# Performance work log

Hardware: AMD Instinct MI355X
Metric: run time of the kernel (lower is better)

The kernel has to match this reference:

```python
import jax, jax.numpy as jnp
import numpy as np

S, B, C = 56, 32, 1024
T = 48
H = 1024          # hidden_size_decoder (== context_size C)
EMB = 512
RANK = 128
VOCAB = 32000


def setup_inputs() -> dict:
    key = jax.random.key(0)
    ks = jax.random.split(key, 16)
    w = 0.05
    inp = {
        "encoded": jax.random.normal(ks[0], (S, B, C), jnp.float32),
        "encoder_state": jax.random.normal(ks[1], (2, B, H), jnp.float32) * 0.1,
        "tgt_tokens": jax.random.randint(ks[2], (B, T), 0, VOCAB),
        "enc_lens": jax.random.randint(ks[3], (B,), S // 2, S + 1).astype(jnp.int32),
        "tgt_lens": jax.random.randint(ks[4], (B,), T // 2, T + 1).astype(jnp.int32),
        "E": jax.random.normal(ks[5], (VOCAB, RANK), jnp.float32) * w,
        "P": jax.random.normal(ks[6], (RANK, EMB), jnp.float32) * w,
        "W0": jax.random.normal(ks[7], (EMB + C, 4 * H), jnp.float32) * w,
        "U0": jax.random.normal(ks[8], (H, 4 * H), jnp.float32) * w,
        "b0": jnp.zeros((4 * H,), jnp.float32),
        "W1": jax.random.normal(ks[9], (H, 4 * H), jnp.float32) * w,
        "U1": jax.random.normal(ks[10], (H, 4 * H), jnp.float32) * w,
        "b1": jnp.zeros((4 * H,), jnp.float32),
        "Wo": jax.random.normal(ks[11], (H + C, EMB), jnp.float32) * w,
        "bo": jnp.zeros((EMB,), jnp.float32),
    }
    return inp


def _lstm_cell(x, h, c, W, U, b):
    gates = x @ W + h @ U + b                      # [B, 4H]
    i, f, g, o = jnp.split(gates, 4, axis=-1)      # torch LSTMCell gate order
    c_new = jax.nn.sigmoid(f) * c + jax.nn.sigmoid(i) * jnp.tanh(g)
    h_new = jax.nn.sigmoid(o) * jnp.tanh(c_new)
    return h_new, c_new


def reference(encoded, encoder_state, tgt_tokens, enc_lens, tgt_lens,
              E, P, W0, U0, b0, W1, U1, b1, Wo, bo):
    # encoded: [S, B, C] (padded encoder outputs), encoder_state: [L=2, B, H]
    enc_b = jnp.transpose(encoded, (1, 0, 2))                 # [B, S, C]
    enc_mask = jnp.arange(S)[None, :] >= enc_lens[:, None]    # [B, S] True = pad

    # factorized embedding lookup (dropout p=0)
    emb = (E[tgt_tokens] @ P)                                 # [B, T, EMB]
    emb_t = jnp.transpose(emb, (1, 0, 2))[: T - 1]            # [T-1, B, EMB]

    h0 = encoder_state                                        # [2, B, H]
    c0 = jnp.zeros_like(encoder_state)
    ctx0 = jnp.zeros((B, C), encoded.dtype)

    def step(carry, x_emb):
        h, c, ctx = carry
        x = jnp.concatenate([x_emb, ctx], axis=-1)            # [B, EMB+C]
        h0n, c0n = _lstm_cell(x, h[0], c[0], W0, U0, b0)
        h1n, c1n = _lstm_cell(h0n, h[1], c[1], W1, U1, b1)
        query = h1n                                           # no context projection
        scores = jnp.einsum("bsc,bc->bs", enc_b, query)       # [B, S]
        scores = jnp.where(enc_mask, -jnp.inf, scores)
        p_att = jax.nn.softmax(scores, axis=-1)
        ctx_new = jnp.einsum("bs,bsc->bc", p_att, enc_b)      # [B, C]
        return (jnp.stack([h0n, h1n]), jnp.stack([c0n, c1n]), ctx_new), (h1n, ctx_new)

    _, (decs, ctxs) = jax.lax.scan(step, (h0, c0, ctx0), emb_t)  # each [T-1, B, *]

    feats = jnp.concatenate([decs, ctxs], axis=-1)            # [T-1, B, H+C]
    hproj = jnp.tanh(feats @ Wo + bo)                          # [T-1, B, EMB]
    logits = (hproj @ P.T) @ E.T                               # [T-1, B, VOCAB]

    labels = tgt_tokens[:, 1:].T                               # [T-1, B]
    logp = jax.nn.log_softmax(logits, axis=-1)
    nll = -jnp.take_along_axis(logp, labels[..., None], axis=-1)[..., 0]
    valid = jnp.arange(T - 1)[:, None] < (tgt_lens[None, :] - 1)  # step t predicts token t+1
    loss = jnp.sum(jnp.where(valid, nll, 0.0))                 # CrossEntropyLoss(reduction='sum')
    return loss
```

## Files before the change

kernel.cpp:

```cpp
#include <hip/hip_runtime.h>
#include <math.h>

#define S_   56
#define B_   32
#define C_   1024
#define T_   48
#define TS   47
#define H_   1024
#define EMB_ 512
#define RANK_ 128
#define VOCAB_ 32000
#define G4   4096
#define NBLK 256

using bf16x8 = __attribute__((ext_vector_type(8))) __bf16;
using f32x4  = __attribute__((ext_vector_type(4))) float;

__device__ __forceinline__ float sigmoidf_(float x){ return 1.0f/(1.0f+expf(-x)); }
__device__ __forceinline__ float b2f(__bf16 x){ return (float)x; }
__device__ __forceinline__ f32x4 z4(){ f32x4 z = {0.f,0.f,0.f,0.f}; return z; }

#define AG __HIP_MEMORY_SCOPE_AGENT
__device__ __forceinline__ void stc_u64(void* p, unsigned long long v){
  __hip_atomic_store((unsigned long long*)p, v, __ATOMIC_RELAXED, AG);
}
__device__ __forceinline__ void stc_bf16(__bf16* p, __bf16 v){
  union { __bf16 b; unsigned short s; } t; t.b = v;
  __hip_atomic_store((unsigned short*)p, t.s, __ATOMIC_RELAXED, AG);
}

struct RedShared {
  float red[4][2][16][18];
};
struct AttnShared {
  union { float hS[1024]; float cred[3][128][8]; } u;
  float sS[64];
  float pS[64];
};
union alignas(16) SharedU { RedShared r; AttnShared a; };

__device__ __forceinline__ void bar_arrive(unsigned* bars, int bi, unsigned e){
  asm volatile("s_waitcnt vmcnt(0)" ::: "memory");
  __syncthreads();
  if (threadIdx.x == 0){
    unsigned* grp = bars + 32*(1 + (bi & 15));
    unsigned old = __hip_atomic_fetch_add(grp, 1u, __ATOMIC_RELAXED, AG);
    if (old == 16u*e - 1u)
      __hip_atomic_fetch_add(bars, 1u, __ATOMIC_RELAXED, AG);
  }
}
__device__ __forceinline__ void bar_wait(unsigned* bars, unsigned e){
  if (threadIdx.x == 0){
    while (__hip_atomic_load(bars, __ATOMIC_RELAXED, AG) < 16u*e)
      __builtin_amdgcn_s_sleep(1);
  }
  __syncthreads();
  asm volatile("" ::: "memory");
}
__device__ __forceinline__ void flag_wait(unsigned* cc, unsigned tgt){
  if (threadIdx.x == 0){
    while (__hip_atomic_load(cc, __ATOMIC_RELAXED, AG) < tgt)
      __builtin_amdgcn_s_sleep(1);
  }
  __syncthreads();
  asm volatile("" ::: "memory");
}

__global__ void k_init(const float* __restrict__ es, __bf16* h0bm1, __bf16* fm1,
                       unsigned* bars){
  int i = blockIdx.x*blockDim.x + threadIdx.x;
  if (i < 32*H_){
    int b = i >> 10, j = i & 1023;
    h0bm1[(size_t)b*1024 + j]       = (__bf16)es[i];
    fm1[(size_t)b*2048 + j]         = (__bf16)es[32*H_ + i];
    fm1[(size_t)b*2048 + 1024 + j]  = (__bf16)0.0f;
  }
  if (i < 1024) bars[i] = 0u;
}

__global__ void k_cvt(const float* __restrict__ src, __bf16* __restrict__ dst, int n){
  int i = (blockIdx.x*blockDim.x + threadIdx.x)*4;
  if (i < n){
    float4 v = *(const float4*)(src + i);
    dst[i+0]=(__bf16)v.x; dst[i+1]=(__bf16)v.y; dst[i+2]=(__bf16)v.z; dst[i+3]=(__bf16)v.w;
  }
}

__global__ void k_embed(const float* __restrict__ E, const float* __restrict__ P,
                        const int* __restrict__ tok, __bf16* __restrict__ embb){
  int blk = blockIdx.x;
  int t = blk >> 5, b = blk & 31, tid = threadIdx.x;
  __shared__ float er[RANK_];
  int tk = tok[b*T_ + t];
  er[tid] = E[(size_t)tk*RANK_ + tid];
  __syncthreads();
  float4 acc = {0.f,0.f,0.f,0.f};
  int e = tid*4;
  for (int r2 = 0; r2 < RANK_; r2++){
    float ev = er[r2];
    float4 p = *(const float4*)(P + (size_t)r2*EMB_ + e);
    acc.x += ev*p.x; acc.y += ev*p.y; acc.z += ev*p.z; acc.w += ev*p.w;
  }
  size_t o = (size_t)blk*EMB_ + e;
  embb[o+0]=(__bf16)acc.x; embb[o+1]=(__bf16)acc.y;
  embb[o+2]=(__bf16)acc.z; embb[o+3]=(__bf16)acc.w;
}

__global__ void k_pack2(const float* __restrict__ W, int K1, const float* __restrict__ U,
                        __bf16* __restrict__ dst, int NCH){
  int ch = blockIdx.x;
  int g  = blockIdx.y >> 2;
  int band = blockIdx.y & 3;
  int tid = threadIdx.x;
  __shared__ __bf16 Tl[32][264];
  {
    int r = tid>>3, cs = tid&7;
    int kk = ch*32 + r;
    const float* src = (kk < K1) ? (W + (size_t)kk*G4 + g*1024 + band*256 + cs*32)
                                 : (U + (size_t)(kk-K1)*G4 + g*1024 + band*256 + cs*32);
    #pragma unroll
    for (int u=0;u<8;u++){
      float4 v = *(const float4*)(src + u*4);
      Tl[r][cs*32+u*4+0]=(__bf16)v.x; Tl[r][cs*32+u*4+1]=(__bf16)v.y;
      Tl[r][cs*32+u*4+2]=(__bf16)v.z; Tl[r][cs*32+u*4+3]=(__bf16)v.w;
    }
  }
  __syncthreads();
  int bil = tid>>2, aq = tid&3;
  int bi = band*64 + bil;
  #pragma unroll
  for (int q=0;q<4;q++){
    __bf16 o8[8];
    #pragma unroll
    for (int i=0;i<8;i++) o8[i] = Tl[aq*8+i][bil*4+q];
    int lane = aq*16 + g*4 + q;
    *(bf16x8*)(dst + (((size_t)bi*NCH + ch)*64 + lane)*8) = *(bf16x8*)o8;
  }
}

__global__ void k_packB(const float* __restrict__ src, __bf16* __restrict__ dst,
                        int K, int N, int tr){
  int kk0 = blockIdx.x*32, j0 = blockIdx.y*16, lane = threadIdx.x;
  int am = lane&15, aq = lane>>4;
  int j = j0 + am;
  __bf16 o8[8];
  #pragma unroll
  for (int i=0;i<8;i++){
    int k = kk0 + aq*8 + i;
    float v = tr ? src[(size_t)j*K + k] : src[(size_t)k*N + j];
    o8[i] = (__bf16)v;
  }
  int NCH = K/32, jt = j0>>4, ch = kk0>>5;
  *(bf16x8*)(dst + (((size_t)jt*NCH + ch)*64 + lane)*8) = *(bf16x8*)o8;
}

template<int NC>
__device__ __forceinline__ void accum(f32x4& acc0, f32x4& acc1,
    const __bf16* __restrict__ abase, int rs, const __bf16* wlds,
    int ch0, int am, int aq, int lane)
{
  const __bf16* a0p = abase + (size_t)am*rs + aq*8;
  const __bf16* a1p = abase + (size_t)(am+16)*rs + aq*8;
  const __bf16* wl  = wlds + (size_t)lane*8;
  #pragma unroll
  for (int c=0;c<NC;c++){
    int ch = ch0 + c;
    bf16x8 a0 = *(const bf16x8*)(a0p + (size_t)ch*32);
    bf16x8 a1 = *(const bf16x8*)(a1p + (size_t)ch*32);
    bf16x8 w  = *(const bf16x8*)(wl  + (size_t)ch*512);
    acc0 = __builtin_amdgcn_mfma_f32_16x16x32_bf16(a0, w, acc0, 0, 0, 0);
    acc1 = __builtin_amdgcn_mfma_f32_16x16x32_bf16(a1, w, acc1, 0, 0, 0);
  }
}

__device__ __forceinline__ void reduce_cell(SharedU& su, const f32x4& acc0, const f32x4& acc1,
    int bi, int tid, const float* __restrict__ bias, float& creg,
    __bf16* __restrict__ hout, int stride)
{
  int kw = tid>>6, lane = tid&63, am = lane&15, aq = lane>>4;
  if (kw >= 4){
    #pragma unroll
    for (int rg=0;rg<4;rg++){
      su.r.red[kw-4][0][aq*4+rg][am] = acc0[rg];
      su.r.red[kw-4][1][aq*4+rg][am] = acc1[rg];
    }
  }
  __syncthreads();
  if (kw < 4){
    #pragma unroll
    for (int rg=0;rg<4;rg++){
      su.r.red[kw][0][aq*4+rg][am] += acc0[rg];
      su.r.red[kw][1][aq*4+rg][am] += acc1[rg];
    }
  }
  __syncthreads();
  if (tid < 128){
    int b = tid>>2, q = tid&3;
    int mt = b>>4, r = b&15;
    float G0=0.f, G1=0.f, G2=0.f, G3=0.f;
    #pragma unroll
    for (int w2=0; w2<4; w2++){
      G0 += su.r.red[w2][mt][r][q];
      G1 += su.r.red[w2][mt][r][4+q];
      G2 += su.r.red[w2][mt][r][8+q];
      G3 += su.r.red[w2][mt][r][12+q];
    }
    int j = bi*4 + q;
    float gi = G0 + bias[j];
    float gf = G1 + bias[1024 + j];
    float gg = G2 + bias[2048 + j];
    float go = G3 + bias[3072 + j];
    float ii = sigmoidf_(gi), ff = sigmoidf_(gf), gv = tanhf(gg), oo = sigmoidf_(go);
    float cv = ff*creg + ii*gv;
    float hv = oo*tanhf(cv);
    creg = cv;
    stc_bf16(hout + (size_t)b*stride + j, (__bf16)hv);
  }
}

__device__ __forceinline__ void attn_block(AttnShared& sa, int b, int tid,
    const __bf16* __restrict__ encb, const int* __restrict__ enc_lens,
    __bf16* __restrict__ fbt)
{
  if (tid < 128){
    bf16x8 h8 = *(const bf16x8*)(fbt + (size_t)b*2048 + tid*8);
    #pragma unroll
    for (int u=0;u<8;u++) sa.u.hS[tid*8+u] = b2f(h8[u]);
  }
  __syncthreads();
  int w = tid >> 6, lane = tid & 63;
  for (int s = w; s < S_; s += 8){
    const __bf16* er = encb + ((size_t)s*32 + b)*C_;
    float a = 0.f;
    #pragma unroll
    for (int half = 0; half < 2; half++){
      int k = lane*8 + half*512;
      bf16x8 e8 = *(const bf16x8*)(er + k);
      #pragma unroll
      for (int u=0;u<8;u++) a += b2f(e8[u]) * sa.u.hS[k+u];
    }
    #pragma unroll
    for (int off=32; off>0; off>>=1) a += __shfl_down(a, off);
    if (lane == 0) sa.sS[s] = a;
  }
  __syncthreads();
  if (tid < 64){
    int len = enc_lens[b];
    float sc = (tid < len && tid < S_) ? sa.sS[tid] : -1e30f;
    float m = sc;
    #pragma unroll
    for (int off=32; off>0; off>>=1) m = fmaxf(m, __shfl_xor(m, off));
    float e = expf(sc - m);
    float ssum = e;
    #pragma unroll
    for (int off=32; off>0; off>>=1) ssum += __shfl_xor(ssum, off);
    sa.pS[tid] = e / ssum;
  }
  __syncthreads();
  int cg = tid & 127, sg = tid >> 7;
  float a8[8];
  #pragma unroll
  for (int i=0;i<8;i++) a8[i] = 0.f;
  for (int s = sg; s < S_; s += 4){
    float p = sa.pS[s];
    bf16x8 e8 = *(const bf16x8*)(encb + ((size_t)s*32 + b)*C_ + cg*8);
    #pragma unroll
    for (int i=0;i<8;i++) a8[i] += p * b2f(e8[i]);
  }
  if (sg > 0){
    #pragma unroll
    for (int i=0;i<8;i++) sa.u.cred[sg-1][cg][i] = a8[i];
  }
  __syncthreads();
  if (sg == 0){
    union { __bf16 bb[8]; unsigned long long u[2]; } cu;
    #pragma unroll
    for (int i=0;i<8;i++){
      float v = a8[i] + sa.u.cred[0][cg][i] + sa.u.cred[1][cg][i] + sa.u.cred[2][cg][i];
      cu.bb[i] = (__bf16)v;
    }
    stc_u64(fbt + (size_t)b*2048 + 1024 + cg*8,     cu.u[0]);
    stc_u64(fbt + (size_t)b*2048 + 1024 + cg*8 + 4, cu.u[1]);
  }
}

__global__ __launch_bounds__(512) void k_loop(
    const __bf16* __restrict__ WP0, const __bf16* __restrict__ WP1,
    const float* __restrict__ b0, const float* __restrict__ b1,
    __bf16* __restrict__ h0b,
    __bf16* __restrict__ featsb,
    const __bf16* __restrict__ embb,
    const __bf16* __restrict__ encb, const int* __restrict__ enc_lens,
    unsigned* bars)
{
  __shared__ __bf16 wB0[80*512];
  __shared__ __bf16 wB1[64*512];
  __shared__ SharedU su;
  int bi = blockIdx.x, tid = threadIdx.x;
  int kw = tid>>6, lane = tid&63, am = lane&15, aq = lane>>4;
  unsigned* ctxcnt = bars + 768;

  {
    const bf16x8* g0 = (const bf16x8*)(WP0 + (size_t)bi*80*512);
    const bf16x8* g1 = (const bf16x8*)(WP1 + (size_t)bi*64*512);
    bf16x8* l0 = (bf16x8*)wB0;
    bf16x8* l1 = (bf16x8*)wB1;
    for (int idx = tid; idx < 80*64; idx += 512) l0[idx] = g0[idx];
    for (int idx = tid; idx < 64*64; idx += 512) l1[idx] = g1[idx];
  }
  __syncthreads();

  float c0r = 0.f, c1r = 0.f;
  f32x4 g00 = z4(), g01 = z4(), g10 = z4(), g11 = z4();

  accum<2>(g00, g01, embb,                     512,  wB0, kw*2,      am, aq, lane);
  accum<4>(g00, g01, h0b - 32768 - 1536,       1024, wB0, 48+kw*4,   am, aq, lane);

  unsigned e = 0;
  for (int t = 0; t < TS; t++){
    const __bf16* fprev = featsb + ((size_t)(t-1))*65536;
    __bf16* h0t = h0b + (size_t)t*32768;
    __bf16* ft  = featsb + (size_t)t*65536;

    flag_wait(ctxcnt, 32u*t);
    accum<4>(g00, g01, fprev + 512, 2048, wB0, 16+kw*4, am, aq, lane);
    reduce_cell(su, g00, g01, bi, tid, b0, c0r, h0t, 1024);
    g00 = z4(); g01 = z4();
    bar_arrive(bars, bi, ++e);
    accum<4>(g10, g11, fprev - 1024, 2048, wB1, 32+kw*4, am, aq, lane);
    bar_wait(bars, e);

    accum<4>(g10, g11, h0t, 1024, wB1, kw*4, am, aq, lane);
    reduce_cell(su, g10, g11, bi, tid, b1, c1r, ft, 2048);
    g10 = z4(); g11 = z4();
    bar_arrive(bars, bi, ++e);
    if (t + 1 < TS){
      accum<2>(g00, g01, embb + (size_t)(t+1)*16384, 512,  wB0, kw*2,    am, aq, lane);
      accum<4>(g00, g01, h0t - 1536,                 1024, wB0, 48+kw*4, am, aq, lane);
    }
    bar_wait(bars, e);

    if (bi < 32){
      attn_block(su.a, bi, tid, encb, enc_lens, ft);
      asm volatile("s_waitcnt vmcnt(0)" ::: "memory");
      __syncthreads();
      if (tid == 0) __hip_atomic_fetch_add(ctxcnt, 1u, __ATOMIC_RELAXED, AG);
    }
  }
}

__global__ __launch_bounds__(256) void k_hproj_mfma(
    const __bf16* __restrict__ fb, const __bf16* __restrict__ WoP,
    const float* __restrict__ bo, __bf16* __restrict__ hpb)
{
  int nt = blockIdx.x, jb = blockIdx.y, tid = threadIdx.x;
  int w = tid>>6, lane = tid&63;
  int mt = w&1, jw = w>>1;
  int am = lane&15, aq = lane>>4;
  const __bf16* aRow = fb + ((size_t)(nt*32 + mt*16 + am))*2048 + aq*8;
  int jt = jb*2 + jw;
  const __bf16* bptr = WoP + ((size_t)jt*64)*512 + lane*8;
  f32x4 acc = {0,0,0,0};
  bf16x8 ar0 = *(const bf16x8*)(aRow);
  bf16x8 br0 = *(const bf16x8*)(bptr);
  bf16x8 ar1 = *(const bf16x8*)(aRow + 32);
  bf16x8 br1 = *(const bf16x8*)(bptr + 512);
  for (int ch = 0; ch < 64; ch += 2){
    bf16x8 a0 = ar0, b0 = br0, a1 = ar1, b1 = br1;
    if (ch + 2 < 64){
      ar0 = *(const bf16x8*)(aRow + (ch+2)*32);
      br0 = *(const bf16x8*)(bptr + (size_t)(ch+2)*512);
      ar1 = *(const bf16x8*)(aRow + (ch+3)*32);
      br1 = *(const bf16x8*)(bptr + (size_t)(ch+3)*512);
    }
    acc = __builtin_amdgcn_mfma_f32_16x16x32_bf16(a0, b0, acc, 0, 0, 0);
    acc = __builtin_amdgcn_mfma_f32_16x16x32_bf16(a1, b1, acc, 0, 0, 0);
  }
  int jcol = jb*32 + jw*16 + am;
  float bv = bo[jcol];
  #pragma unroll
  for (int rg=0; rg<4; rg++){
    int m = nt*32 + mt*16 + aq*4 + rg;
    hpb[(size_t)m*512 + jcol] = (__bf16)tanhf(acc[rg] + bv);
  }
}

__global__ __launch_bounds__(256) void k_rproj_mfma(
    const __bf16* __restrict__ hpb, const __bf16* __restrict__ PP,
    __bf16* __restrict__ rb)
{
  int nt = blockIdx.x, jb = blockIdx.y, tid = threadIdx.x;
  int w = tid>>6, lane = tid&63;
  int mt = w&1, jw = w>>1;
  int am = lane&15, aq = lane>>4;
  const __bf16* aRow = hpb + ((size_t)(nt*32 + mt*16 + am))*512 + aq*8;
  int jt = jb*2 + jw;
  const __bf16* bptr = PP + ((size_t)jt*16)*512 + lane*8;
  f32x4 acc = {0,0,0,0};
  #pragma unroll
  for (int ch = 0; ch < 16; ch++){
    bf16x8 a = *(const bf16x8*)(aRow + ch*32);
    bf16x8 b = *(const bf16x8*)(bptr + (size_t)ch*512);
    acc = __builtin_amdgcn_mfma_f32_16x16x32_bf16(a, b, acc, 0, 0, 0);
  }
  int jcol = jb*32 + jw*16 + am;
  #pragma unroll
  for (int rg=0; rg<4; rg++){
    int m = nt*32 + mt*16 + aq*4 + rg;
    rb[(size_t)m*RANK_ + jcol] = (__bf16)acc[rg];
  }
}

__global__ __launch_bounds__(256) void k_vocab2(
    const __bf16* __restrict__ rb, const __bf16* __restrict__ Eb,
    const int* __restrict__ tok,
    float* __restrict__ mpart, float* __restrict__ lpart,
    float* __restrict__ lablog)
{
  int vc = blockIdx.x, tid = threadIdx.x;
  int w = tid>>6, lane = tid&63;
  int am = lane&15, aq = lane>>4;
  int vb = vc*128 + w*32;
  bf16x8 bfr[2][4];
  #pragma unroll
  for (int vt=0; vt<2; vt++)
    #pragma unroll
    for (int ks=0; ks<4; ks++)
      bfr[vt][ks] = *(const bf16x8*)(Eb + ((size_t)(vb + vt*16 + am))*RANK_ + ks*32 + aq*8);

  __shared__ float redM[4][32], redL[4][32];
  for (int nt = 0; nt < TS; nt++){
    f32x4 acc[2][2] = {{{0,0,0,0},{0,0,0,0}},{{0,0,0,0},{0,0,0,0}}};
    #pragma unroll
    for (int mt=0; mt<2; mt++){
      #pragma unroll
      for (int ks=0; ks<4; ks++){
        bf16x8 a = *(const bf16x8*)(rb + ((size_t)(nt*32 + mt*16 + am))*RANK_ + ks*32 + aq*8);
        acc[mt][0] = __builtin_amdgcn_mfma_f32_16x16x32_bf16(a, bfr[0][ks], acc[mt][0], 0,0,0);
        acc[mt][1] = __builtin_amdgcn_mfma_f32_16x16x32_bf16(a, bfr[1][ks], acc[mt][1], 0,0,0);
      }
    }
    #pragma unroll
    for (int mt=0; mt<2; mt++){
      #pragma unroll
      for (int rg=0; rg<4; rg++){
        int row = mt*16 + aq*4 + rg;
        int n = nt*32 + row;
        int lbl = tok[row*T_ + nt + 1];
        float v0 = acc[mt][0][rg], v1 = acc[mt][1][rg];
        if (vb + am == lbl)      lablog[n] = v0;
        if (vb + 16 + am == lbl) lablog[n] = v1;
        float m = fmaxf(v0, v1);
        #pragma unroll
        for (int off=1; off<16; off<<=1) m = fmaxf(m, __shfl_xor(m, off));
        float l = expf(v0 - m) + expf(v1 - m);
        #pragma unroll
        for (int off=1; off<16; off<<=1) l += __shfl_xor(l, off);
        if (am == 0){ redM[w][row] = m; redL[w][row] = l; }
      }
    }
    __syncthreads();
    if (tid < 32){
      float M = fmaxf(fmaxf(redM[0][tid], redM[1][tid]), fmaxf(redM[2][tid], redM[3][tid]));
      float L = 0.f;
      #pragma unroll
      for (int ww=0; ww<4; ww++) L += redL[ww][tid]*expf(redM[ww][tid] - M);
      mpart[(size_t)(nt*32 + tid)*250 + vc] = M;
      lpart[(size_t)(nt*32 + tid)*250 + vc] = L;
    }
    __syncthreads();
  }
}

__global__ void k_loss1(const float* __restrict__ mpart, const float* __restrict__ lpart,
                        const float* __restrict__ lablog, const int* __restrict__ tgt_lens,
                        float* __restrict__ tpart){
  int t = blockIdx.x, tid = threadIdx.x;
  int row = tid >> 3, cq = tid & 7;
  int n = t*32 + row;
  float m = -1e30f;
  for (int c = cq; c < 250; c += 8) m = fmaxf(m, mpart[(size_t)n*250 + c]);
  #pragma unroll
  for (int off=1; off<8; off<<=1) m = fmaxf(m, __shfl_xor(m, off));
  float l = 0.f;
  for (int c = cq; c < 250; c += 8) l += lpart[(size_t)n*250 + c]*expf(mpart[(size_t)n*250 + c] - m);
  #pragma unroll
  for (int off=1; off<8; off<<=1) l += __shfl_xor(l, off);
  __shared__ float red[32];
  if (cq == 0)
    red[row] = (t < tgt_lens[row] - 1) ? (m + logf(l) - lablog[n]) : 0.f;
  __syncthreads();
  if (tid == 0){
    float s = 0.f;
    #pragma unroll
    for (int i=0;i<32;i++) s += red[i];
    tpart[t] = s;
  }
}

__global__ void k_loss2(const float* __restrict__ tpart, float* __restrict__ out){
  int tid = threadIdx.x;
  float v = (tid < TS) ? tpart[tid] : 0.f;
  #pragma unroll
  for (int off=32; off>0; off>>=1) v += __shfl_down(v, off);
  if (tid == 0) out[0] = v;
}

extern "C" void kernel_launch(void* const* d_in, const int* in_sizes, int n_in,
                              void* d_out, int out_size, void* d_ws, size_t ws_size,
                              hipStream_t stream){
  const float* enc      = (const float*)d_in[0];
  const float* es       = (const float*)d_in[1];
  const int*   tok      = (const int*)  d_in[2];
  const int*   enc_lens = (const int*)  d_in[3];
  const int*   tgt_lens = (const int*)  d_in[4];
  const float* E        = (const float*)d_in[5];
  const float* P        = (const float*)d_in[6];
  const float* W0       = (const float*)d_in[7];
  const float* U0       = (const float*)d_in[8];
  const float* b0       = (const float*)d_in[9];
  const float* W1       = (const float*)d_in[10];
  const float* U1       = (const float*)d_in[11];
  const float* b1       = (const float*)d_in[12];
  const float* Wo       = (const float*)d_in[13];
  const float* bo       = (const float*)d_in[14];
  float* out = (float*)d_out;

  float* fb = (float*)d_ws;
  size_t fo = 0;
  float* mpart = fb + fo; fo += (size_t)TS*32*250;
  float* lpart = fb + fo; fo += (size_t)TS*32*250;
  float* lab   = fb + fo; fo += (size_t)TS*32;
  float* tpart = fb + fo; fo += 64;
  unsigned* bars = (unsigned*)(fb + fo); fo += 1024;
  __bf16* bb = (__bf16*)(fb + fo);
  size_t bo2 = 0;
  __bf16* WP0    = bb + bo2; bo2 += (size_t)4096*2560;
  __bf16* WP1    = bb + bo2; bo2 += (size_t)4096*2048;
  __bf16* encb   = bb + bo2; bo2 += (size_t)S_*32*C_;
  __bf16* embb   = bb + bo2; bo2 += (size_t)TS*32*EMB_;
  __bf16* rbuf   = bb + bo2; bo2 += (size_t)TS*32*RANK_;
  __bf16* WoP    = bb + bo2; bo2 += (size_t)2048*512;
  __bf16* PP     = bb + bo2; bo2 += (size_t)512*128;
  __bf16* featsb0= bb + bo2; bo2 += (size_t)(TS+1)*32*2048;
  __bf16* hpb    = bb + bo2; bo2 += (size_t)TS*32*EMB_;
  __bf16* h0b0   = bb + bo2; bo2 += (size_t)(TS+1)*32*1024;
  __bf16* Eb     = WP0;

  __bf16* featsb = featsb0 + (size_t)32*2048;
  __bf16* h0b    = h0b0 + (size_t)32*1024;

  k_init<<<128, 256, 0, stream>>>(es, h0b0, featsb0, bars);
  k_cvt<<<(S_*32*C_/4 + 255)/256, 256, 0, stream>>>(enc, encb, S_*32*C_);
  k_embed<<<TS*32, 128, 0, stream>>>(E, P, tok, embb);
  k_pack2<<<dim3(80,16), 256, 0, stream>>>(W0, 1536, U0, WP0, 80);
  k_pack2<<<dim3(64,16), 256, 0, stream>>>(W1, 1024, U1, WP1, 64);
  k_packB<<<dim3(64,32), 64, 0, stream>>>(Wo, WoP, 2048, 512, 0);
  k_packB<<<dim3(16,8), 64, 0, stream>>>(P, PP, 512, 128, 1);

  k_loop<<<NBLK, 512, 0, stream>>>(WP0, WP1, b0, b1, h0b, featsb,
                                   embb, encb, enc_lens, bars);

  k_cvt<<<(VOCAB_*RANK_/4 + 255)/256, 256, 0, stream>>>(E, Eb, VOCAB_*RANK_);

  k_hproj_mfma<<<dim3(TS,16), 256, 0, stream>>>(featsb, WoP, bo, hpb);
  k_rproj_mfma<<<dim3(TS,4), 256, 0, stream>>>(hpb, PP, rbuf);
  k_vocab2<<<250, 256, 0, stream>>>(rbuf, Eb, tok, mpart, lpart, lab);
  k_loss1<<<TS, 256, 0, stream>>>(mpart, lpart, lab, tgt_lens, tpart);
  k_loss2<<<1, 64, 0, stream>>>(tpart, out);
}
```

Baseline: 1.478 ms.

## Precompute encoder·W0ctx projection and defer context vectors out of the recurrent loop

Uses linearity: ctx@W0ctx = p_att·(enc@W0ctx), so enc@W0ctx is precomputed once by a new MFMA kernel (k_encw) into a per-block packed layout. The recurrent loop now only writes attention probabilities; layer-0 gates add a 56-length dot product against the precomputed projection instead of a 1024-wide context GEMM slice. The full context vectors needed later for the output projection are rebuilt after the loop by a separate k_ctx kernel. This shrinks the per-step serial work (the context weighted sum and part of the layer-0 GEMM) and the LDS weight footprint. In exchange it adds a large precompute GEMM, extra per-step global reads of the encWp slice and probabilities, and bf16 rounding of the projected values.

```diff
diff --git a/kernel.cpp b/kernel.cpp
--- a/kernel.cpp
+++ b/kernel.cpp
@@ -21,19 +21,20 @@
 __device__ __forceinline__ f32x4 z4(){ f32x4 z = {0.f,0.f,0.f,0.f}; return z; }
 
 #define AG __HIP_MEMORY_SCOPE_AGENT
-__device__ __forceinline__ void stc_u64(void* p, unsigned long long v){
-  __hip_atomic_store((unsigned long long*)p, v, __ATOMIC_RELAXED, AG);
-}
 __device__ __forceinline__ void stc_bf16(__bf16* p, __bf16 v){
   union { __bf16 b; unsigned short s; } t; t.b = v;
   __hip_atomic_store((unsigned short*)p, t.s, __ATOMIC_RELAXED, AG);
 }
+__device__ __forceinline__ void stc_f32(float* p, float v){
+  __hip_atomic_store(p, v, __ATOMIC_RELAXED, AG);
+}
 
 struct RedShared {
   float red[4][2][16][18];
+  float pS2[2048];
 };
 struct AttnShared {
-  union { float hS[1024]; float cred[3][128][8]; } u;
+  float hS[1024];
   float sS[64];
   float pS[64];
 };
@@ -67,14 +68,14 @@
 }
 
 __global__ void k_init(const float* __restrict__ es, __bf16* h0bm1, __bf16* fm1,
-                       unsigned* bars){
+                       float* pbufm1, unsigned* bars){
   int i = blockIdx.x*blockDim.x + threadIdx.x;
   if (i < 32*H_){
     int b = i >> 10, j = i & 1023;
-    h0bm1[(size_t)b*1024 + j]       = (__bf16)es[i];
-    fm1[(size_t)b*2048 + j]         = (__bf16)es[32*H_ + i];
-    fm1[(size_t)b*2048 + 1024 + j]  = (__bf16)0.0f;
-  }
+    h0bm1[(size_t)b*1024 + j] = (__bf16)es[i];
+    fm1[(size_t)b*2048 + j]   = (__bf16)es[32*H_ + i];
+  }
+  if (i < 2048) pbufm1[i] = 0.f;
   if (i < 1024) bars[i] = 0u;
 }
 
@@ -106,18 +107,18 @@
   embb[o+2]=(__bf16)acc.z; embb[o+3]=(__bf16)acc.w;
 }
 
-__global__ void k_pack2(const float* __restrict__ W, int K1, const float* __restrict__ U,
-                        __bf16* __restrict__ dst, int NCH){
-  int ch = blockIdx.x;
+__global__ void k_pack2(const float* __restrict__ A, int K1, const float* __restrict__ Bsrc,
+                        __bf16* __restrict__ dst, int NCH, int ch0){
+  int bx = blockIdx.x;
   int g  = blockIdx.y >> 2;
   int band = blockIdx.y & 3;
   int tid = threadIdx.x;
   __shared__ __bf16 Tl[32][264];
   {
     int r = tid>>3, cs = tid&7;
-    int kk = ch*32 + r;
-    const float* src = (kk < K1) ? (W + (size_t)kk*G4 + g*1024 + band*256 + cs*32)
-                                 : (U + (size_t)(kk-K1)*G4 + g*1024 + band*256 + cs*32);
+    int kk = bx*32 + r;
+    const float* src = (kk < K1) ? (A + (size_t)kk*G4 + g*1024 + band*256 + cs*32)
+                                 : (Bsrc + (size_t)(kk-K1)*G4 + g*1024 + band*256 + cs*32);
     #pragma unroll
     for (int u=0;u<8;u++){
       float4 v = *(const float4*)(src + u*4);
@@ -128,6 +129,7 @@
   __syncthreads();
   int bil = tid>>2, aq = tid&3;
   int bi = band*64 + bil;
+  int ch = ch0 + bx;
   #pragma unroll
   for (int q=0;q<4;q++){
     __bf16 o8[8];
@@ -152,6 +154,64 @@
   }
   int NCH = K/32, jt = j0>>4, ch = kk0>>5;
   *(bf16x8*)(dst + (((size_t)jt*NCH + ch)*64 + lane)*8) = *(bf16x8*)o8;
+}
+
+__global__ __launch_bounds__(256) void k_encw(
+    const float* __restrict__ W0, const __bf16* __restrict__ encb,
+    __bf16* __restrict__ encWp)
+{
+  __shared__ __bf16 Bl[8*16*64*8];
+  int mg = blockIdx.x, ng = blockIdx.y, tid = threadIdx.x;
+  int w = tid>>6, lane = tid&63, am = lane&15, aq = lane>>4;
+  int m0 = mg*128, j0 = ng*128;
+  f32x4 acc[8][2];
+  #pragma unroll
+  for (int i=0;i<8;i++){ acc[i][0]=z4(); acc[i][1]=z4(); }
+  for (int h=0; h<2; h++){
+    __syncthreads();
+    for (int idx = tid; idx < 8192; idx += 256){
+      int row = idx >> 4, seg = idx & 15;
+      const float* src = W0 + (size_t)(512 + h*512 + row)*G4 + j0 + seg*8;
+      float4 v0 = *(const float4*)src;
+      float4 v1 = *(const float4*)(src+4);
+      int ch = row >> 5, r5 = row & 31;
+      int aq2 = r5 >> 3, i8 = r5 & 7;
+      int jtl = seg >> 1, amb = (seg & 1)*8;
+      __bf16* d = Bl + (((size_t)jtl*16 + ch)*64 + aq2*16 + amb)*8 + i8;
+      float vv[8] = {v0.x,v0.y,v0.z,v0.w,v1.x,v1.y,v1.z,v1.w};
+      #pragma unroll
+      for (int u=0;u<8;u++) d[u*8] = (__bf16)vv[u];
+    }
+    __syncthreads();
+    int jt2 = w*2;
+    #pragma unroll
+    for (int mt=0; mt<8; mt++){
+      const __bf16* ap = encb + (size_t)(m0 + mt*16 + am)*1024 + h*512 + aq*8;
+      #pragma unroll
+      for (int ch=0; ch<16; ch++){
+        bf16x8 a  = *(const bf16x8*)(ap + ch*32);
+        bf16x8 bA = *(const bf16x8*)(Bl + (((size_t)jt2*16 + ch)*64 + lane)*8);
+        bf16x8 bB = *(const bf16x8*)(Bl + (((size_t)(jt2+1)*16 + ch)*64 + lane)*8);
+        acc[mt][0] = __builtin_amdgcn_mfma_f32_16x16x32_bf16(a, bA, acc[mt][0], 0,0,0);
+        acc[mt][1] = __builtin_amdgcn_mfma_f32_16x16x32_bf16(a, bB, acc[mt][1], 0,0,0);
+      }
+    }
+  }
+  #pragma unroll
+  for (int mt=0; mt<8; mt++){
+    #pragma unroll
+    for (int jj=0; jj<2; jj++){
+      int jcol = j0 + (w*2+jj)*16 + am;
+      int biW = (jcol & 1023) >> 2;
+      int gq  = ((jcol >> 10) << 2) | (jcol & 3);
+      #pragma unroll
+      for (int rg=0; rg<4; rg++){
+        int m = m0 + mt*16 + aq*4 + rg;
+        int b = m & 31, s = m >> 5;
+        encWp[((size_t)(biW*32 + b)*16 + gq)*56 + s] = (__bf16)acc[mt][jj][rg];
+      }
+    }
+  }
 }
 
 template<int NC>
@@ -173,9 +233,10 @@
   }
 }
 
+template<bool GCTX>
 __device__ __forceinline__ void reduce_cell(SharedU& su, const f32x4& acc0, const f32x4& acc1,
     int bi, int tid, const float* __restrict__ bias, float& creg,
-    __bf16* __restrict__ hout, int stride)
+    __bf16* __restrict__ hout, int stride, const __bf16* __restrict__ encWb)
 {
   int kw = tid>>6, lane = tid&63, am = lane&15, aq = lane>>4;
   if (kw >= 4){
@@ -204,6 +265,24 @@
       G1 += su.r.red[w2][mt][r][4+q];
       G2 += su.r.red[w2][mt][r][8+q];
       G3 += su.r.red[w2][mt][r][12+q];
+    }
+    if (GCTX){
+      const __bf16* eb = encWb + (size_t)b*896 + q*56;
+      float d0=0.f,d1=0.f,d2=0.f,d3=0.f;
+      #pragma unroll
+      for (int s0=0; s0<56; s0+=8){
+        bf16x8 e0 = *(const bf16x8*)(eb + s0);
+        bf16x8 e1 = *(const bf16x8*)(eb + 224 + s0);
+        bf16x8 e2 = *(const bf16x8*)(eb + 448 + s0);
+        bf16x8 e3 = *(const bf16x8*)(eb + 672 + s0);
+        #pragma unroll
+        for (int u=0;u<8;u++){
+          float p = su.r.pS2[b*64 + s0 + u];
+          d0 += p*b2f(e0[u]); d1 += p*b2f(e1[u]);
+          d2 += p*b2f(e2[u]); d3 += p*b2f(e3[u]);
+        }
+      }
+      G0 += d0; G1 += d1; G2 += d2; G3 += d3;
     }
     int j = bi*4 + q;
     float gi = G0 + bias[j];
@@ -220,12 +299,12 @@
 
 __device__ __forceinline__ void attn_block(AttnShared& sa, int b, int tid,
     const __bf16* __restrict__ encb, const int* __restrict__ enc_lens,
-    __bf16* __restrict__ fbt)
+    const __bf16* __restrict__ fbt, float* __restrict__ pbt)
 {
   if (tid < 128){
     bf16x8 h8 = *(const bf16x8*)(fbt + (size_t)b*2048 + tid*8);
     #pragma unroll
-    for (int u=0;u<8;u++) sa.u.hS[tid*8+u] = b2f(h8[u]);
+    for (int u=0;u<8;u++) sa.hS[tid*8+u] = b2f(h8[u]);
   }
   __syncthreads();
   int w = tid >> 6, lane = tid & 63;
@@ -237,7 +316,7 @@
       int k = lane*8 + half*512;
       bf16x8 e8 = *(const bf16x8*)(er + k);
       #pragma unroll
-      for (int u=0;u<8;u++) a += b2f(e8[u]) * sa.u.hS[k+u];
+      for (int u=0;u<8;u++) a += b2f(e8[u]) * sa.hS[k+u];
     }
     #pragma unroll
     for (int off=32; off>0; off>>=1) a += __shfl_down(a, off);
@@ -254,58 +333,33 @@
     float ssum = e;
     #pragma unroll
     for (int off=32; off>0; off>>=1) ssum += __shfl_xor(ssum, off);
-    sa.pS[tid] = e / ssum;
-  }
-  __syncthreads();
-  int cg = tid & 127, sg = tid >> 7;
-  float a8[8];
-  #pragma unroll
-  for (int i=0;i<8;i++) a8[i] = 0.f;
-  for (int s = sg; s < S_; s += 4){
-    float p = sa.pS[s];
-    bf16x8 e8 = *(const bf16x8*)(encb + ((size_t)s*32 + b)*C_ + cg*8);
-    #pragma unroll
-    for (int i=0;i<8;i++) a8[i] += p * b2f(e8[i]);
-  }
-  if (sg > 0){
-    #pragma unroll
-    for (int i=0;i<8;i++) sa.u.cred[sg-1][cg][i] = a8[i];
-  }
-  __syncthreads();
-  if (sg == 0){
-    union { __bf16 bb[8]; unsigned long long u[2]; } cu;
-    #pragma unroll
-    for (int i=0;i<8;i++){
-      float v = a8[i] + sa.u.cred[0][cg][i] + sa.u.cred[1][cg][i] + sa.u.cred[2][cg][i];
-      cu.bb[i] = (__bf16)v;
-    }
-    stc_u64(fbt + (size_t)b*2048 + 1024 + cg*8,     cu.u[0]);
-    stc_u64(fbt + (size_t)b*2048 + 1024 + cg*8 + 4, cu.u[1]);
+    if (tid < 56) stc_f32(pbt + b*64 + tid, e / ssum);
   }
 }
 
 __global__ __launch_bounds__(512) void k_loop(
     const __bf16* __restrict__ WP0, const __bf16* __restrict__ WP1,
     const float* __restrict__ b0, const float* __restrict__ b1,
-    __bf16* __restrict__ h0b,
-    __bf16* __restrict__ featsb,
+    __bf16* __restrict__ h0b, __bf16* __restrict__ featsb,
     const __bf16* __restrict__ embb,
     const __bf16* __restrict__ encb, const int* __restrict__ enc_lens,
+    const __bf16* __restrict__ encWp, float* __restrict__ pbuf0,
     unsigned* bars)
 {
-  __shared__ __bf16 wB0[80*512];
+  __shared__ __bf16 wB0[48*512];
   __shared__ __bf16 wB1[64*512];
   __shared__ SharedU su;
   int bi = blockIdx.x, tid = threadIdx.x;
   int kw = tid>>6, lane = tid&63, am = lane&15, aq = lane>>4;
   unsigned* ctxcnt = bars + 768;
+  const __bf16* encWb = encWp + (size_t)bi*28672;
 
   {
-    const bf16x8* g0 = (const bf16x8*)(WP0 + (size_t)bi*80*512);
+    const bf16x8* g0 = (const bf16x8*)(WP0 + (size_t)bi*48*512);
     const bf16x8* g1 = (const bf16x8*)(WP1 + (size_t)bi*64*512);
     bf16x8* l0 = (bf16x8*)wB0;
     bf16x8* l1 = (bf16x8*)wB1;
-    for (int idx = tid; idx < 80*64; idx += 512) l0[idx] = g0[idx];
+    for (int idx = tid; idx < 48*64; idx += 512) l0[idx] = g0[idx];
     for (int idx = tid; idx < 64*64; idx += 512) l1[idx] = g1[idx];
   }
   __syncthreads();
@@ -313,8 +367,8 @@
   float c0r = 0.f, c1r = 0.f;
   f32x4 g00 = z4(), g01 = z4(), g10 = z4(), g11 = z4();
 
-  accum<2>(g00, g01, embb,                     512,  wB0, kw*2,      am, aq, lane);
-  accum<4>(g00, g01, h0b - 32768 - 1536,       1024, wB0, 48+kw*4,   am, aq, lane);
+  accum<2>(g00, g01, embb,                 512,  wB0, kw*2,    am, aq, lane);
+  accum<4>(g00, g01, h0b - 32768 - 512,    1024, wB0, 16+kw*4, am, aq, lane);
 
   unsigned e = 0;
   for (int t = 0; t < TS; t++){
@@ -323,29 +377,59 @@
     __bf16* ft  = featsb + (size_t)t*65536;
 
     flag_wait(ctxcnt, 32u*t);
-    accum<4>(g00, g01, fprev + 512, 2048, wB0, 16+kw*4, am, aq, lane);
-    reduce_cell(su, g00, g01, bi, tid, b0, c0r, h0t, 1024);
+    {
+      const float* pprev = pbuf0 + (size_t)t*2048;
+      for (int i = tid; i < 2048; i += 512) su.r.pS2[i] = pprev[i];
+    }
+    reduce_cell<true>(su, g00, g01, bi, tid, b0, c0r, h0t, 1024, encWb);
     g00 = z4(); g01 = z4();
     bar_arrive(bars, bi, ++e);
     accum<4>(g10, g11, fprev - 1024, 2048, wB1, 32+kw*4, am, aq, lane);
     bar_wait(bars, e);
 
     accum<4>(g10, g11, h0t, 1024, wB1, kw*4, am, aq, lane);
-    reduce_cell(su, g10, g11, bi, tid, b1, c1r, ft, 2048);
+    reduce_cell<false>(su, g10, g11, bi, tid, b1, c1r, ft, 2048, (const __bf16*)nullptr);
     g10 = z4(); g11 = z4();
     bar_arrive(bars, bi, ++e);
     if (t + 1 < TS){
       accum<2>(g00, g01, embb + (size_t)(t+1)*16384, 512,  wB0, kw*2,    am, aq, lane);
-      accum<4>(g00, g01, h0t - 1536,                 1024, wB0, 48+kw*4, am, aq, lane);
+      accum<4>(g00, g01, h0t - 512,                  1024, wB0, 16+kw*4, am, aq, lane);
     }
     bar_wait(bars, e);
 
     if (bi < 32){
-      attn_block(su.a, bi, tid, encb, enc_lens, ft);
+      attn_block(su.a, bi, tid, encb, enc_lens, ft, pbuf0 + (size_t)(t+1)*2048);
       asm volatile("s_waitcnt vmcnt(0)" ::: "memory");
       __syncthreads();
       if (tid == 0) __hip_atomic_fetch_add(ctxcnt, 1u, __ATOMIC_RELAXED, AG);
     }
+  }
+}
+
+__global__ __launch_bounds__(256) void k_ctx(
+    const __bf16* __restrict__ encb, const float* __restrict__ pbuf0,
+    __bf16* __restrict__ featsb)
+{
+  __shared__ __bf16 encL[56*1024];
+  __shared__ float pL[64];
+  int b = blockIdx.x, tid = threadIdx.x;
+  for (int i = tid*8; i < 56*1024; i += 256*8){
+    int s = i >> 10, c = i & 1023;
+    *(bf16x8*)(encL + i) = *(const bf16x8*)(encb + ((size_t)s*32 + b)*C_ + c);
+  }
+  for (int t = 0; t < TS; t++){
+    __syncthreads();
+    if (tid < 56) pL[tid] = pbuf0[(size_t)(t+1)*2048 + b*64 + tid];
+    __syncthreads();
+    int c0 = tid*4;
+    float a0=0.f,a1=0.f,a2=0.f,a3=0.f;
+    for (int s=0;s<56;s++){
+      float p = pL[s];
+      const __bf16* er = encL + s*1024 + c0;
+      a0 += p*b2f(er[0]); a1 += p*b2f(er[1]); a2 += p*b2f(er[2]); a3 += p*b2f(er[3]);
+    }
+    __bf16* d = featsb + (size_t)t*65536 + (size_t)b*2048 + 1024 + c0;
+    d[0]=(__bf16)a0; d[1]=(__bf16)a1; d[2]=(__bf16)a2; d[3]=(__bf16)a3;
   }
 }
 
@@ -528,40 +612,45 @@
 
   float* fb = (float*)d_ws;
   size_t fo = 0;
+  unsigned* bars = (unsigned*)(fb + fo); fo += 1024;
+  float* pbuf0 = fb + fo; fo += (size_t)(TS+1)*2048;
   float* mpart = fb + fo; fo += (size_t)TS*32*250;
   float* lpart = fb + fo; fo += (size_t)TS*32*250;
   float* lab   = fb + fo; fo += (size_t)TS*32;
   float* tpart = fb + fo; fo += 64;
-  unsigned* bars = (unsigned*)(fb + fo); fo += 1024;
   __bf16* bb = (__bf16*)(fb + fo);
   size_t bo2 = 0;
-  __bf16* WP0    = bb + bo2; bo2 += (size_t)4096*2560;
-  __bf16* WP1    = bb + bo2; bo2 += (size_t)4096*2048;
+  __bf16* WP0    = bb + bo2; bo2 += (size_t)256*48*512;
+  __bf16* WP1    = bb + bo2; bo2 += (size_t)256*64*512;
   __bf16* encb   = bb + bo2; bo2 += (size_t)S_*32*C_;
   __bf16* embb   = bb + bo2; bo2 += (size_t)TS*32*EMB_;
+  __bf16* featsb0= bb + bo2; bo2 += (size_t)(TS+1)*32*2048;
+  __bf16* h0b0   = bb + bo2; bo2 += (size_t)(TS+1)*32*1024;
+  __bf16* encWp  = bb + bo2; bo2 += (size_t)256*32*16*56;
   __bf16* rbuf   = bb + bo2; bo2 += (size_t)TS*32*RANK_;
-  __bf16* WoP    = bb + bo2; bo2 += (size_t)2048*512;
-  __bf16* PP     = bb + bo2; bo2 += (size_t)512*128;
-  __bf16* featsb0= bb + bo2; bo2 += (size_t)(TS+1)*32*2048;
   __bf16* hpb    = bb + bo2; bo2 += (size_t)TS*32*EMB_;
-  __bf16* h0b0   = bb + bo2; bo2 += (size_t)(TS+1)*32*1024;
   __bf16* Eb     = WP0;
+  __bf16* WoP    = WP1;
+  __bf16* PP     = WP1 + (size_t)2048*512;
 
   __bf16* featsb = featsb0 + (size_t)32*2048;
   __bf16* h0b    = h0b0 + (size_t)32*1024;
 
-  k_init<<<128, 256, 0, stream>>>(es, h0b0, featsb0, bars);
+  k_init<<<128, 256, 0, stream>>>(es, h0b0, featsb0, pbuf0, bars);
   k_cvt<<<(S_*32*C_/4 + 255)/256, 256, 0, stream>>>(enc, encb, S_*32*C_);
   k_embed<<<TS*32, 128, 0, stream>>>(E, P, tok, embb);
-  k_pack2<<<dim3(80,16), 256, 0, stream>>>(W0, 1536, U0, WP0, 80);
-  k_pack2<<<dim3(64,16), 256, 0, stream>>>(W1, 1024, U1, WP1, 64);
+  k_pack2<<<dim3(16,16), 256, 0, stream>>>(W0, 512,  W0, WP0, 48, 0);
+  k_pack2<<<dim3(32,16), 256, 0, stream>>>(U0, 1024, U0, WP0, 48, 16);
+  k_pack2<<<dim3(64,16), 256, 0, stream>>>(W1, 1024, U1, WP1, 64, 0);
+  k_encw<<<dim3(14,32), 256, 0, stream>>>(W0, encb, encWp);
+
+  k_loop<<<NBLK, 512, 0, stream>>>(WP0, WP1, b0, b1, h0b, featsb,
+                                   embb, encb, enc_lens, encWp, pbuf0, bars);
+
+  k_cvt<<<(VOCAB_*RANK_/4 + 255)/256, 256, 0, stream>>>(E, Eb, VOCAB_*RANK_);
   k_packB<<<dim3(64,32), 64, 0, stream>>>(Wo, WoP, 2048, 512, 0);
   k_packB<<<dim3(16,8), 64, 0, stream>>>(P, PP, 512, 128, 1);
-
-  k_loop<<<NBLK, 512, 0, stream>>>(WP0, WP1, b0, b1, h0b, featsb,
-                                   embb, encb, enc_lens, bars);
-
-  k_cvt<<<(VOCAB_*RANK_/4 + 255)/256, 256, 0, stream>>>(E, Eb, VOCAB_*RANK_);
+  k_ctx<<<32, 256, 0, stream>>>(encb, pbuf0, featsb);
 
   k_hproj_mfma<<<dim3(TS,16), 256, 0, stream>>>(featsb, WoP, bo, hpb);
   k_rproj_mfma<<<dim3(TS,4), 256, 0, stream>>>(hpb, PP, rbuf);
```

Result: slower. 1.812 ms (+22.6%).
